# Performance work log

Hardware: AMD Instinct MI355X
Metric: run time of the kernel (lower is better)

Reference implementation:

```python
import jax, jax.numpy as jnp
import numpy as np

V, E, H, N, T, L = 32000, 1024, 1024, 64, 32, 196


def setup_inputs() -> dict:
    key = jax.random.key(0)
    ks = jax.random.split(key, 12)
    s = 0.02
    return {
        "inputs": jax.random.randint(ks[0], (N, T), 0, V, dtype=jnp.int32),
        "img_features": jax.random.normal(ks[1], (N, L, H), dtype=jnp.float32),
        "emb": jax.random.normal(ks[2], (V, E), dtype=jnp.float32) * s,
        "w_ih1": jax.random.normal(ks[3], (4 * H, E), dtype=jnp.float32) * s,
        "w_hh1": jax.random.normal(ks[4], (4 * H, H), dtype=jnp.float32) * s,
        "b_ih1": jax.random.normal(ks[5], (4 * H,), dtype=jnp.float32) * s,
        "b_hh1": jax.random.normal(ks[6], (4 * H,), dtype=jnp.float32) * s,
        "w_ih2": jax.random.normal(ks[7], (4 * H, 2 * H), dtype=jnp.float32) * s,
        "w_hh2": jax.random.normal(ks[8], (4 * H, H), dtype=jnp.float32) * s,
        "b_ih2": jax.random.normal(ks[9], (4 * H,), dtype=jnp.float32) * s,
        "b_hh2": jax.random.normal(ks[10], (4 * H,), dtype=jnp.float32) * s,
    }


def _lstm_cell(x, h, c, w_ih, w_hh, b_ih, b_hh):
    # PyTorch LSTMCell: gates ordered i, f, g, o
    g = x @ w_ih.T + b_ih + h @ w_hh.T + b_hh
    i, f, gg, o = jnp.split(g, 4, axis=-1)
    c_new = jax.nn.sigmoid(f) * c + jax.nn.sigmoid(i) * jnp.tanh(gg)
    h_new = jax.nn.sigmoid(o) * jnp.tanh(c_new)
    return h_new, c_new


def reference(inputs, img_features, emb, w_ih1, w_hh1, b_ih1, b_hh1,
              w_ih2, w_hh2, b_ih2, b_hh2):
    n, t = inputs.shape
    hdim = w_hh1.shape[1]
    embedded = emb[inputs]                      # (N, T, E)
    # faithful to original: .view(T, N, -1) is a reshape, NOT a transpose
    xs = embedded.reshape(t, n, -1)             # (T, N, E)

    def step(carry, x_t):
        h1, c1, h2, c2 = carry
        h1, c1 = _lstm_cell(x_t, h1, c1, w_ih1, w_hh1, b_ih1, b_hh1)
        # attention: raw dot-product weights (no softmax in original)
        alpha = jnp.einsum('nd,nld->nl', h1, img_features)   # (N, L)
        v_att = jnp.einsum('nl,nld->nd', alpha, img_features) # (N, D)
        x2 = jnp.concatenate([v_att, h1], axis=1)             # (N, 2H)
        h2, c2 = _lstm_cell(x2, h2, c2, w_ih2, w_hh2, b_ih2, b_hh2)
        return (h1, c1, h2, c2), h2

    zeros = jnp.zeros((n, hdim), dtype=img_features.dtype)
    init = (zeros, zeros, zeros, zeros)
    _, hs = jax.lax.scan(step, init, xs)        # (T, N, H)
    # faithful to original: cat along dim 0 then .view(N, T, -1) == reshape
    return hs.reshape(n, t, -1)
```

## Files before the change

### kernel.cpp

```cpp
#include <hip/hip_runtime.h>
#include <math.h>

typedef __attribute__((ext_vector_type(8))) short bf16x8;
typedef __attribute__((ext_vector_type(4))) short short4v;
typedef __attribute__((ext_vector_type(4))) float f32x4;

__device__ __forceinline__ float sigm(float x) { return 1.f / (1.f + expf(-x)); }

__device__ __forceinline__ float bf2f(short x) {
    unsigned u = ((unsigned)(unsigned short)x) << 16;
    float f; __builtin_memcpy(&f, &u, 4); return f;
}
__device__ __forceinline__ short f2bf(float f) {
    unsigned u; __builtin_memcpy(&u, &f, 4);
    unsigned r = (u + 0x7fffu + ((u >> 16) & 1u)) >> 16;
    return (short)r;
}

__device__ __forceinline__ unsigned sys_ld(const unsigned* p) {
    return __hip_atomic_load(p, __ATOMIC_RELAXED, __HIP_MEMORY_SCOPE_SYSTEM);
}
__device__ __forceinline__ void sys_st(unsigned* p, unsigned v) {
    __hip_atomic_store(p, v, __ATOMIC_RELAXED, __HIP_MEMORY_SCOPE_SYSTEM);
}

#define OFF_C1      0u
#define OFF_H1HI    786432u
#define OFF_H1LO    5111808u
#define OFF_H1F     9437184u
#define OFF_X0HI    17825792u
#define OFF_X0LO    22020096u
#define OFF_B1      26214400u
#define OFF_B2      26230784u
#define OFF_WHH1HI  26247168u
#define OFF_WHH1LO  34635776u
#define OFF_WIH1HI  43024384u
#define OFF_WIH1LO  51412992u
#define OFF_WHH2HI  59801600u
#define OFF_WVHI    68190208u
#define OFF_WVLO    76578816u
#define OFF_WH2HI   84967424u
#define OFF_X12     93356032u

__global__ __launch_bounds__(256) void zero_ws(float4* __restrict__ p) {
    int i = blockIdx.x * 256 + threadIdx.x;
    p[i] = make_float4(0.f, 0.f, 0.f, 0.f);
}

__global__ __launch_bounds__(256) void zero_slots(unsigned* __restrict__ p) {
    int i = blockIdx.x * 256 + threadIdx.x;
    __hip_atomic_store(p + i, 0u, __ATOMIC_RELAXED, __HIP_MEMORY_SCOPE_SYSTEM);
}

__global__ __launch_bounds__(256) void perm_w_split(const float* __restrict__ src,
                                                    short* __restrict__ hi,
                                                    short* __restrict__ lo,
                                                    int rs, int co) {
    int idx = blockIdx.x * 256 + threadIdx.x;
    int jp = idx >> 8;
    int kq = idx & 255;
    int jsrc = (jp & 3) * 1024 + (jp >> 2);
    float4 v = *(const float4*)(src + (size_t)jsrc * rs + co + kq * 4);
    float a[4] = {v.x, v.y, v.z, v.w};
    short4v h, l;
    #pragma unroll
    for (int e = 0; e < 4; e++) {
        short q = f2bf(a[e]);
        h[e] = q;
        l[e] = f2bf(a[e] - bf2f(q));
    }
    *(short4v*)(hi + (size_t)jp * 1024 + kq * 4) = h;
    *(short4v*)(lo + (size_t)jp * 1024 + kq * 4) = l;
}

__global__ __launch_bounds__(256) void bias_prep(
    const float* __restrict__ bi1, const float* __restrict__ bh1,
    const float* __restrict__ bi2, const float* __restrict__ bh2,
    float* __restrict__ b1p, float* __restrict__ b2p) {
    int jp = blockIdx.x * 256 + threadIdx.x;
    int j = (jp & 3) * 1024 + (jp >> 2);
    b1p[jp] = bi1[j] + bh1[j];
    b2p[jp] = bi2[j] + bh2[j];
}

__global__ __launch_bounds__(256) void gather_x0_split(
    const int* __restrict__ tokens, const float* __restrict__ emb,
    short* __restrict__ hi, short* __restrict__ lo) {
    int idx = blockIdx.x * 256 + threadIdx.x;
    int p = idx >> 8;
    int k0 = (idx & 255) * 4;
    int tok = tokens[p];
    float4 v = *(const float4*)(emb + (size_t)tok * 1024 + k0);
    float a[4] = {v.x, v.y, v.z, v.w};
    short4v h, l;
    #pragma unroll
    for (int e = 0; e < 4; e++) {
        short q = f2bf(a[e]);
        h[e] = q;
        l[e] = f2bf(a[e] - bf2f(q));
    }
    *(short4v*)(hi + (size_t)p * 1024 + k0) = h;
    *(short4v*)(lo + (size_t)p * 1024 + k0) = l;
}

__global__ __launch_bounds__(256) void big_gemm(
    const short* __restrict__ A0, const short* __restrict__ A1s,
    const short* __restrict__ A2s, const short* __restrict__ A3s,
    const short* __restrict__ B0, const short* __restrict__ B1s,
    const short* __restrict__ B2s, const short* __restrict__ B3s,
    const float* __restrict__ bias, float* __restrict__ C, int K) {
    __shared__ short As[128 * 40];
    __shared__ short Bs[128 * 40];
    int tid = threadIdx.x;
    int n0 = blockIdx.x * 128;
    int m0 = blockIdx.y * 128;
    int lane = tid & 63, w = tid >> 6;
    int wm = (w >> 1) * 64, wn = (w & 1) * 64;
    int quad = lane >> 4, l16 = lane & 15;
    int srow = tid >> 2;
    int skc = (tid & 3) * 8;

    f32x4 acc[4][4];
    f32x4 z4 = {0.f, 0.f, 0.f, 0.f};
    #pragma unroll
    for (int i = 0; i < 4; i++)
        #pragma unroll
        for (int j = 0; j < 4; j++) acc[i][j] = z4;

    for (int k0 = 0; k0 < K; k0 += 32) {
        int seg = k0 >> 10;
        const short* Ab = (seg == 0) ? A0 : (seg == 1) ? A1s : (seg == 2) ? A2s : A3s;
        const short* Bb = (seg == 0) ? B0 : (seg == 1) ? B1s : (seg == 2) ? B2s : B3s;
        int kk = (k0 & 1023) + skc;
        const short* ga = Ab + (size_t)(m0 + srow) * 1024 + kk;
        const short* gb = Bb + (size_t)(n0 + srow) * 1024 + kk;
        bf16x8 av0 = *(const bf16x8*)ga;
        bf16x8 av1 = *(const bf16x8*)(ga + 64 * 1024);
        bf16x8 bv0 = *(const bf16x8*)gb;
        bf16x8 bv1 = *(const bf16x8*)(gb + 64 * 1024);
        __syncthreads();
        *(bf16x8*)&As[srow * 40 + skc] = av0;
        *(bf16x8*)&As[(srow + 64) * 40 + skc] = av1;
        *(bf16x8*)&Bs[srow * 40 + skc] = bv0;
        *(bf16x8*)&Bs[(srow + 64) * 40 + skc] = bv1;
        __syncthreads();
        bf16x8 af[4], bfr[4];
        #pragma unroll
        for (int im = 0; im < 4; im++)
            af[im] = *(const bf16x8*)&As[(wm + im * 16 + l16) * 40 + quad * 8];
        #pragma unroll
        for (int in = 0; in < 4; in++)
            bfr[in] = *(const bf16x8*)&Bs[(wn + in * 16 + l16) * 40 + quad * 8];
        #pragma unroll
        for (int im = 0; im < 4; im++)
            #pragma unroll
            for (int in = 0; in < 4; in++)
                acc[im][in] = __builtin_amdgcn_mfma_f32_16x16x32_bf16(
                    af[im], bfr[in], acc[im][in], 0, 0, 0);
    }
    #pragma unroll
    for (int in = 0; in < 4; in++) {
        int j = n0 + wn + in * 16 + l16;
        float bsv = bias[j];
        #pragma unroll
        for (int im = 0; im < 4; im++) {
            #pragma unroll
            for (int r = 0; r < 4; r++) {
                int p = m0 + wm + im * 16 + quad * 4 + r;
                C[(size_t)p * 4096 + j] = acc[im][in][r] + bsv;
            }
        }
    }
}

__global__ __launch_bounds__(256, 1) void lstm1_fused(
    const short* __restrict__ Whi, const short* __restrict__ Wlo,
    const float* __restrict__ X12,
    short* __restrict__ H1hi, short* __restrict__ H1lo,
    float* __restrict__ H1f,
    unsigned* __restrict__ arrive) {
    __shared__ short wsh[16 * 1032];
    __shared__ float red[4 * 64 * 16];

    int tid = threadIdx.x;
    int lane = tid & 63, w = tid >> 6;
    int quad = lane >> 4, l16 = lane & 15;
    int g = blockIdx.x;
    int kbase = w * 256;

    for (int i = tid; i < 2048; i += 256) {
        int r = i >> 7;
        int k = (i & 127) * 8;
        *(bf16x8*)&wsh[r * 1032 + k] =
            *(const bf16x8*)(Whi + (size_t)(g * 16 + r) * 1024 + k);
    }

    int s = tid >> 2, dl = tid & 3;
    int d = g * 4 + dl;
    float creg = 0.f;

    __syncthreads();

    const short* bhp = &wsh[l16 * 1032 + kbase + quad * 8];
    const short* blp = Wlo + (size_t)(g * 16 + l16) * 1024 + kbase + quad * 8;
    const float* xgp = X12 + (size_t)s * 4096 + g * 16 + dl * 4;

    float4 xg = *(const float4*)xgp;

    for (int t = 0; t < 32; t++) {
        f32x4 acc[4];
        f32x4 z4 = {0.f, 0.f, 0.f, 0.f};
        acc[0] = z4; acc[1] = z4; acc[2] = z4; acc[3] = z4;

        if (t > 0) {
            const short* ah = H1hi + (size_t)t * 65536 + (size_t)l16 * 1024 + kbase + quad * 8;
            const short* al = H1lo + (size_t)t * 65536 + (size_t)l16 * 1024 + kbase + quad * 8;
            #pragma unroll
            for (int i = 0; i < 8; i++) {
                int k = i * 32;
                bf16x8 Bh = *(const bf16x8*)(bhp + k);
                bf16x8 Bl = *(const bf16x8*)(blp + k);
                #pragma unroll
                for (int mt = 0; mt < 4; mt++) {
                    bf16x8 Ah = *(const bf16x8*)(ah + mt * 16 * 1024 + k);
                    bf16x8 Al = *(const bf16x8*)(al + mt * 16 * 1024 + k);
                    acc[mt] = __builtin_amdgcn_mfma_f32_16x16x32_bf16(Ah, Bh, acc[mt], 0, 0, 0);
                    acc[mt] = __builtin_amdgcn_mfma_f32_16x16x32_bf16(Al, Bh, acc[mt], 0, 0, 0);
                    acc[mt] = __builtin_amdgcn_mfma_f32_16x16x32_bf16(Ah, Bl, acc[mt], 0, 0, 0);
                }
            }
        }
        #pragma unroll
        for (int mt = 0; mt < 4; mt++)
            #pragma unroll
            for (int r = 0; r < 4; r++) {
                int sr = mt * 16 + quad * 4 + r;
                red[(w * 64 + sr) * 16 + l16] = acc[mt][r];
            }
        __syncthreads();

        float gi = 0.f, gf = 0.f, gg = 0.f, go = 0.f;
        #pragma unroll
        for (int w2 = 0; w2 < 4; w2++) {
            const float* rp = &red[(w2 * 64 + s) * 16 + dl * 4];
            gi += rp[0]; gf += rp[1]; gg += rp[2]; go += rp[3];
        }
        gi += xg.x; gf += xg.y; gg += xg.z; go += xg.w;
        float cn = sigm(gf) * creg + sigm(gi) * tanhf(gg);
        creg = cn;
        float hn = sigm(go) * tanhf(cn);
        short q = f2bf(hn);
        short ql = f2bf(hn - bf2f(q));

        unsigned pr = ((unsigned)(unsigned short)q) |
                      (((unsigned)(unsigned short)ql) << 16);
        int lb = lane & ~3;
        unsigned p0 = __shfl(pr, lb + 0, 64);
        unsigned p1 = __shfl(pr, lb + 1, 64);
        unsigned p2 = __shfl(pr, lb + 2, 64);
        unsigned p3 = __shfl(pr, lb + 3, 64);
        if (dl == 0) {
            unsigned long long hi4 =
                (unsigned long long)(p0 & 0xffffu) |
                ((unsigned long long)(p1 & 0xffffu) << 16) |
                ((unsigned long long)(p2 & 0xffffu) << 32) |
                ((unsigned long long)(p3 & 0xffffu) << 48);
            unsigned long long lo4 =
                (unsigned long long)(p0 >> 16) |
                ((unsigned long long)(p1 >> 16) << 16) |
                ((unsigned long long)(p2 >> 16) << 32) |
                ((unsigned long long)(p3 >> 16) << 48);
            __hip_atomic_store(
                (unsigned long long*)&H1hi[(size_t)(t + 1) * 65536 + s * 1024 + g * 4],
                hi4, __ATOMIC_RELAXED, __HIP_MEMORY_SCOPE_AGENT);
            __hip_atomic_store(
                (unsigned long long*)&H1lo[(size_t)(t + 1) * 65536 + s * 1024 + g * 4],
                lo4, __ATOMIC_RELAXED, __HIP_MEMORY_SCOPE_AGENT);
        }
        __syncthreads();
        if (t != 31) {
            unsigned tgt = (unsigned)(t + 1);
            if (tid == 0) sys_st(arrive + g, tgt);
            H1f[(size_t)t * 65536 + s * 1024 + d] = hn;
            xg = *(const float4*)(xgp + (size_t)(t + 1) * 262144);
            if (tid < 64) {
                const unsigned* p = arrive + tid * 4;
                for (;;) {
                    unsigned a = sys_ld(p + 0), b = sys_ld(p + 1);
                    unsigned c = sys_ld(p + 2), e = sys_ld(p + 3);
                    int ok = (a >= tgt) && (b >= tgt) && (c >= tgt) && (e >= tgt);
                    if (__all(ok)) break;
                    __builtin_amdgcn_s_sleep(4);
                }
            }
            __syncthreads();
            asm volatile("" ::: "memory");
        } else {
            H1f[(size_t)t * 65536 + s * 1024 + d] = hn;
        }
    }
}

__global__ __launch_bounds__(256, 1) void lstm2_fused(
    const short* __restrict__ W, const float* __restrict__ X12,
    short* __restrict__ H2,
    float* __restrict__ out,
    unsigned* __restrict__ arrive) {
    __shared__ short wsh[16 * 1032];
    __shared__ float red[4 * 64 * 16];

    int tid = threadIdx.x;
    int lane = tid & 63, w = tid >> 6;
    int quad = lane >> 4, l16 = lane & 15;
    int g = blockIdx.x;
    int kbase = w * 256;

    for (int i = tid; i < 2048; i += 256) {
        int r = i >> 7;
        int k = (i & 127) * 8;
        *(bf16x8*)&wsh[r * 1032 + k] =
            *(const bf16x8*)(W + (size_t)(g * 16 + r) * 1024 + k);
    }

    int s = tid >> 2, dl = tid & 3;
    int d = g * 4 + dl;
    float creg = 0.f;

    __syncthreads();

    const short* bp = &wsh[l16 * 1032 + kbase + quad * 8];
    const float* xgp = X12 + (size_t)s * 4096 + g * 16 + dl * 4;

    float4 xg = *(const float4*)xgp;

    for (int t = 0; t < 32; t++) {
        f32x4 acc[4];
        f32x4 z4 = {0.f, 0.f, 0.f, 0.f};
        acc[0] = z4; acc[1] = z4; acc[2] = z4; acc[3] = z4;

        if (t > 0) {
            const short* ar = H2 + (size_t)t * 65536 + (size_t)l16 * 1024 + kbase + quad * 8;
            #pragma unroll
            for (int i = 0; i < 8; i++) {
                int k = i * 32;
                bf16x8 b = *(const bf16x8*)(bp + k);
                #pragma unroll
                for (int mt = 0; mt < 4; mt++) {
                    bf16x8 a = *(const bf16x8*)(ar + mt * 16 * 1024 + k);
                    acc[mt] = __builtin_amdgcn_mfma_f32_16x16x32_bf16(a, b, acc[mt], 0, 0, 0);
                }
            }
        }
        #pragma unroll
        for (int mt = 0; mt < 4; mt++)
            #pragma unroll
            for (int r = 0; r < 4; r++) {
                int sr = mt * 16 + quad * 4 + r;
                red[(w * 64 + sr) * 16 + l16] = acc[mt][r];
            }
        __syncthreads();

        float gi = 0.f, gf = 0.f, gg = 0.f, go = 0.f;
        #pragma unroll
        for (int w2 = 0; w2 < 4; w2++) {
            const float* rp = &red[(w2 * 64 + s) * 16 + dl * 4];
            gi += rp[0]; gf += rp[1]; gg += rp[2]; go += rp[3];
        }
        gi += xg.x; gf += xg.y; gg += xg.z; go += xg.w;
        float cn = sigm(gf) * creg + sigm(gi) * tanhf(gg);
        creg = cn;
        float hn = sigm(go) * tanhf(cn);

        unsigned pr = (unsigned)(unsigned short)f2bf(hn);
        int lb = lane & ~3;
        unsigned p0 = __shfl(pr, lb + 0, 64);
        unsigned p1 = __shfl(pr, lb + 1, 64);
        unsigned p2 = __shfl(pr, lb + 2, 64);
        unsigned p3 = __shfl(pr, lb + 3, 64);
        if (dl == 0) {
            unsigned long long h4 =
                (unsigned long long)(p0 & 0xffffu) |
                ((unsigned long long)(p1 & 0xffffu) << 16) |
                ((unsigned long long)(p2 & 0xffffu) << 32) |
                ((unsigned long long)(p3 & 0xffffu) << 48);
            __hip_atomic_store(
                (unsigned long long*)&H2[(size_t)(t + 1) * 65536 + s * 1024 + g * 4],
                h4, __ATOMIC_RELAXED, __HIP_MEMORY_SCOPE_AGENT);
        }
        __syncthreads();
        if (t != 31) {
            unsigned tgt = (unsigned)(t + 1);
            if (tid == 0) sys_st(arrive + g, tgt);
            out[(size_t)t * 65536 + s * 1024 + d] = hn;
            xg = *(const float4*)(xgp + (size_t)(t + 1) * 262144);
            if (tid < 64) {
                const unsigned* p = arrive + tid * 4;
                for (;;) {
                    unsigned a = sys_ld(p + 0), b = sys_ld(p + 1);
                    unsigned c = sys_ld(p + 2), e = sys_ld(p + 3);
                    int ok = (a >= tgt) && (b >= tgt) && (c >= tgt) && (e >= tgt);
                    if (__all(ok)) break;
                    __builtin_amdgcn_s_sleep(4);
                }
            }
            __syncthreads();
            asm volatile("" ::: "memory");
        } else {
            out[(size_t)t * 65536 + s * 1024 + d] = hn;
        }
    }
}

__global__ __launch_bounds__(256) void attn_batch(
    const float* __restrict__ H1f, const float* __restrict__ F,
    short* __restrict__ Vhi, short* __restrict__ Vlo) {
    __shared__ float vs[4][4][1024];
    int n = blockIdx.x, tg = blockIdx.y;
    int tid = threadIdx.x, lane = tid & 63, w = tid >> 6;

    float h[4][16];
    #pragma unroll
    for (int tt = 0; tt < 4; tt++) {
        const float* hp = H1f + ((size_t)((tg * 4 + tt) * 64 + n)) * 1024 + lane * 16;
        #pragma unroll
        for (int j = 0; j < 4; j++) {
            float4 v = *(const float4*)(hp + j * 4);
            h[tt][j * 4 + 0] = v.x; h[tt][j * 4 + 1] = v.y;
            h[tt][j * 4 + 2] = v.z; h[tt][j * 4 + 3] = v.w;
        }
    }
    float vacc[4][16];
    #pragma unroll
    for (int tt = 0; tt < 4; tt++)
        #pragma unroll
        for (int j = 0; j < 16; j++) vacc[tt][j] = 0.f;

    const float* Fn = F + ((size_t)n * 196) * 1024 + lane * 16;
    for (int l = w; l < 196; l += 4) {
        const float* fr = Fn + (size_t)l * 1024;
        float f[16];
        #pragma unroll
        for (int j = 0; j < 4; j++) {
            float4 v = *(const float4*)(fr + j * 4);
            f[j * 4 + 0] = v.x; f[j * 4 + 1] = v.y;
            f[j * 4 + 2] = v.z; f[j * 4 + 3] = v.w;
        }
        float p[4] = {0.f, 0.f, 0.f, 0.f};
        #pragma unroll
        for (int tt = 0; tt < 4; tt++)
            #pragma unroll
            for (int j = 0; j < 16; j++) p[tt] += f[j] * h[tt][j];
        #pragma unroll
        for (int off = 32; off > 0; off >>= 1) {
            #pragma unroll
            for (int tt = 0; tt < 4; tt++) p[tt] += __shfl_xor(p[tt], off, 64);
        }
        #pragma unroll
        for (int tt = 0; tt < 4; tt++)
            #pragma unroll
            for (int j = 0; j < 16; j++) vacc[tt][j] += p[tt] * f[j];
    }
    #pragma unroll
    for (int tt = 0; tt < 4; tt++)
        #pragma unroll
        for (int j4 = 0; j4 < 4; j4++) {
            float4 v;
            v.x = vacc[tt][j4 * 4 + 0]; v.y = vacc[tt][j4 * 4 + 1];
            v.z = vacc[tt][j4 * 4 + 2]; v.w = vacc[tt][j4 * 4 + 3];
            *(float4*)&vs[w][tt][lane * 16 + j4 * 4] = v;
        }
    __syncthreads();
    int d0 = tid * 4;
    #pragma unroll
    for (int tt = 0; tt < 4; tt++) {
        float4 a = *(const float4*)&vs[0][tt][d0];
        float4 b = *(const float4*)&vs[1][tt][d0];
        float4 cc = *(const float4*)&vs[2][tt][d0];
        float4 e = *(const float4*)&vs[3][tt][d0];
        float sv[4];
        sv[0] = a.x + b.x + cc.x + e.x;
        sv[1] = a.y + b.y + cc.y + e.y;
        sv[2] = a.z + b.z + cc.z + e.z;
        sv[3] = a.w + b.w + cc.w + e.w;
        short4v b1, b2;
        #pragma unroll
        for (int e2 = 0; e2 < 4; e2++) {
            short q = f2bf(sv[e2]);
            b1[e2] = q;
            b2[e2] = f2bf(sv[e2] - bf2f(q));
        }
        size_t row = ((size_t)(tg * 4 + tt) * 64 + n) * 1024 + d0;
        *(short4v*)(Vhi + row) = b1;
        *(short4v*)(Vlo + row) = b2;
    }
}

extern "C" void kernel_launch(void* const* d_in, const int* in_sizes, int n_in,
                              void* d_out, int out_size, void* d_ws, size_t ws_size,
                              hipStream_t stream) {
    const int*   tokens = (const int*)d_in[0];
    const float* imgf   = (const float*)d_in[1];
    const float* emb    = (const float*)d_in[2];
    const float* w_ih1  = (const float*)d_in[3];
    const float* w_hh1  = (const float*)d_in[4];
    const float* b_ih1  = (const float*)d_in[5];
    const float* b_hh1  = (const float*)d_in[6];
    const float* w_ih2  = (const float*)d_in[7];
    const float* w_hh2  = (const float*)d_in[8];
    const float* b_ih2  = (const float*)d_in[9];
    const float* b_hh2  = (const float*)d_in[10];
    float* out = (float*)d_out;
    char* ws = (char*)d_ws;

    unsigned* arrive1 = (unsigned*)(ws + OFF_C1);
    unsigned* arrive2 = (unsigned*)(ws + OFF_C1 + 4096u);
    short* H1hi   = (short*)(ws + OFF_H1HI);
    short* H1lo   = (short*)(ws + OFF_H1LO);
    float* H1f    = (float*)(ws + OFF_H1F);
    short* H2     = (short*)(ws + OFF_H1F);
    short* X0hi   = (short*)(ws + OFF_X0HI);
    short* X0lo   = (short*)(ws + OFF_X0LO);
    short* Vhi    = (short*)(ws + OFF_X0HI);
    short* Vlo    = (short*)(ws + OFF_X0LO);
    float* bias1p = (float*)(ws + OFF_B1);
    float* bias2p = (float*)(ws + OFF_B2);
    short* whh1hi = (short*)(ws + OFF_WHH1HI);
    short* whh1lo = (short*)(ws + OFF_WHH1LO);
    short* wih1hi = (short*)(ws + OFF_WIH1HI);
    short* wih1lo = (short*)(ws + OFF_WIH1LO);
    short* whh2hi = (short*)(ws + OFF_WHH2HI);
    short* wvhi   = (short*)(ws + OFF_WVHI);
    short* wvlo   = (short*)(ws + OFF_WVLO);
    short* wh2hi  = (short*)(ws + OFF_WH2HI);
    float* X12    = (float*)(ws + OFF_X12);
    short* dump   = (short*)(ws + OFF_X12);

    zero_slots<<<8, 256, 0, stream>>>((unsigned*)(ws + OFF_C1));
    perm_w_split<<<4096, 256, 0, stream>>>(w_hh1, whh1hi, whh1lo, 1024, 0);
    perm_w_split<<<4096, 256, 0, stream>>>(w_ih1, wih1hi, wih1lo, 1024, 0);
    perm_w_split<<<4096, 256, 0, stream>>>(w_hh2, whh2hi, dump, 1024, 0);
    perm_w_split<<<4096, 256, 0, stream>>>(w_ih2, wvhi, wvlo, 2048, 0);
    perm_w_split<<<4096, 256, 0, stream>>>(w_ih2, wh2hi, dump, 2048, 1024);
    bias_prep<<<16, 256, 0, stream>>>(b_ih1, b_hh1, b_ih2, b_hh2, bias1p, bias2p);
    gather_x0_split<<<2048, 256, 0, stream>>>(tokens, emb, X0hi, X0lo);

    big_gemm<<<dim3(32, 16), 256, 0, stream>>>(
        X0hi, X0lo, X0hi, X0hi,
        wih1hi, wih1hi, wih1lo, wih1hi,
        bias1p, X12, 3072);

    lstm1_fused<<<256, 256, 0, stream>>>(
        whh1hi, whh1lo, X12, H1hi, H1lo, H1f, arrive1);

    attn_batch<<<dim3(64, 8), 256, 0, stream>>>(H1f, imgf, Vhi, Vlo);

    big_gemm<<<dim3(32, 16), 256, 0, stream>>>(
        Vhi, Vlo, Vhi, H1hi + 65536,
        wvhi, wvhi, wvlo, wh2hi,
        bias2p, X12, 4096);

    lstm2_fused<<<256, 256, 0, stream>>>(
        whh2hi, X12, H2, out, arrive2);
}
```

Baseline: 1.143 ms.

## Replace all-to-all spin barrier with master-block arrive/release barrier

```diff
diff --git a/kernel.cpp b/kernel.cpp
--- a/kernel.cpp
+++ b/kernel.cpp
@@ -178,7 +178,7 @@
     const float* __restrict__ X12,
     short* __restrict__ H1hi, short* __restrict__ H1lo,
     float* __restrict__ H1f,
-    unsigned* __restrict__ arrive) {
+    unsigned* __restrict__ arrive, unsigned* __restrict__ release) {
     __shared__ short wsh[16 * 1032];
     __shared__ float red[4 * 64 * 16];
 
@@ -280,20 +280,20 @@
         __syncthreads();
         if (t != 31) {
             unsigned tgt = (unsigned)(t + 1);
-            if (tid == 0) sys_st(arrive + g, tgt);
+            if (tid == 0) sys_st(arrive + (size_t)g * 32, tgt);
             H1f[(size_t)t * 65536 + s * 1024 + d] = hn;
             xg = *(const float4*)(xgp + (size_t)(t + 1) * 262144);
-            if (tid < 64) {
-                const unsigned* p = arrive + tid * 4;
-                for (;;) {
-                    unsigned a = sys_ld(p + 0), b = sys_ld(p + 1);
-                    unsigned c = sys_ld(p + 2), e = sys_ld(p + 3);
-                    int ok = (a >= tgt) && (b >= tgt) && (c >= tgt) && (e >= tgt);
-                    if (__all(ok)) break;
-                    __builtin_amdgcn_s_sleep(4);
-                }
-            }
-            __syncthreads();
+            if (g == 0) {
+                const unsigned* my = arrive + (size_t)tid * 32;
+                while (sys_ld(my) < tgt) __builtin_amdgcn_s_sleep(2);
+                __syncthreads();
+                sys_st(release + (size_t)tid * 32, tgt);
+            } else {
+                if (tid == 0)
+                    while (sys_ld(release + (size_t)g * 32) < tgt)
+                        __builtin_amdgcn_s_sleep(2);
+                __syncthreads();
+            }
             asm volatile("" ::: "memory");
         } else {
             H1f[(size_t)t * 65536 + s * 1024 + d] = hn;
@@ -305,7 +305,7 @@
     const short* __restrict__ W, const float* __restrict__ X12,
     short* __restrict__ H2,
     float* __restrict__ out,
-    unsigned* __restrict__ arrive) {
+    unsigned* __restrict__ arrive, unsigned* __restrict__ release) {
     __shared__ short wsh[16 * 1032];
     __shared__ float red[4 * 64 * 16];
 
@@ -390,20 +390,20 @@
         __syncthreads();
         if (t != 31) {
             unsigned tgt = (unsigned)(t + 1);
-            if (tid == 0) sys_st(arrive + g, tgt);
+            if (tid == 0) sys_st(arrive + (size_t)g * 32, tgt);
             out[(size_t)t * 65536 + s * 1024 + d] = hn;
             xg = *(const float4*)(xgp + (size_t)(t + 1) * 262144);
-            if (tid < 64) {
-                const unsigned* p = arrive + tid * 4;
-                for (;;) {
-                    unsigned a = sys_ld(p + 0), b = sys_ld(p + 1);
-                    unsigned c = sys_ld(p + 2), e = sys_ld(p + 3);
-                    int ok = (a >= tgt) && (b >= tgt) && (c >= tgt) && (e >= tgt);
-                    if (__all(ok)) break;
-                    __builtin_amdgcn_s_sleep(4);
-                }
-            }
-            __syncthreads();
+            if (g == 0) {
+                const unsigned* my = arrive + (size_t)tid * 32;
+                while (sys_ld(my) < tgt) __builtin_amdgcn_s_sleep(2);
+                __syncthreads();
+                sys_st(release + (size_t)tid * 32, tgt);
+            } else {
+                if (tid == 0)
+                    while (sys_ld(release + (size_t)g * 32) < tgt)
+                        __builtin_amdgcn_s_sleep(2);
+                __syncthreads();
+            }
             asm volatile("" ::: "memory");
         } else {
             out[(size_t)t * 65536 + s * 1024 + d] = hn;
@@ -512,8 +512,10 @@
     float* out = (float*)d_out;
     char* ws = (char*)d_ws;
 
-    unsigned* arrive1 = (unsigned*)(ws + OFF_C1);
-    unsigned* arrive2 = (unsigned*)(ws + OFF_C1 + 4096u);
+    unsigned* arrive1  = (unsigned*)(ws + OFF_C1);
+    unsigned* release1 = (unsigned*)(ws + OFF_C1 + 32768u);
+    unsigned* arrive2  = (unsigned*)(ws + OFF_C1 + 65536u);
+    unsigned* release2 = (unsigned*)(ws + OFF_C1 + 98304u);
     short* H1hi   = (short*)(ws + OFF_H1HI);
     short* H1lo   = (short*)(ws + OFF_H1LO);
     float* H1f    = (float*)(ws + OFF_H1F);
@@ -535,7 +537,7 @@
     float* X12    = (float*)(ws + OFF_X12);
     short* dump   = (short*)(ws + OFF_X12);
 
-    zero_slots<<<8, 256, 0, stream>>>((unsigned*)(ws + OFF_C1));
+    zero_slots<<<128, 256, 0, stream>>>((unsigned*)(ws + OFF_C1));
     perm_w_split<<<4096, 256, 0, stream>>>(w_hh1, whh1hi, whh1lo, 1024, 0);
     perm_w_split<<<4096, 256, 0, stream>>>(w_ih1, wih1hi, wih1lo, 1024, 0);
     perm_w_split<<<4096, 256, 0, stream>>>(w_hh2, whh2hi, dump, 1024, 0);
@@ -550,7 +552,7 @@
         bias1p, X12, 3072);
 
     lstm1_fused<<<256, 256, 0, stream>>>(
-        whh1hi, whh1lo, X12, H1hi, H1lo, H1f, arrive1);
+        whh1hi, whh1lo, X12, H1hi, H1lo, H1f, arrive1, release1);
 
     attn_batch<<<dim3(64, 8), 256, 0, stream>>>(H1f, imgf, Vhi, Vlo);
 
@@ -560,5 +562,5 @@
         bias2p, X12, 4096);
 
     lstm2_fused<<<256, 256, 0, stream>>>(
-        whh2hi, X12, H2, out, arrive2);
-}
+        whh2hi, X12, H2, out, arrive2, release2);
+}
```

After: 1.052 ms. -7.9%, faster.
